# Optimization experiments

Hardware: AMD Instinct MI355X
Metric: run time of the kernel (lower is better)

Reference implementation:

```python
import jax, jax.numpy as jnp
import numpy as np

B, QL, ML = 8, 128, 1024
QS, KS, H = 512, 512, 256


def setup_inputs() -> dict:
    key = jax.random.key(0)
    ks = jax.random.split(key, 10)
    query = jax.random.normal(ks[0], (B, QL, QS), dtype=jnp.float32)
    memory = jax.random.normal(ks[1], (B, ML, KS), dtype=jnp.float32)
    mask = jax.random.bernoulli(ks[2], 0.1, (B, ML))
    mask = mask.at[:, 0].set(False)  # ensure at least one valid position per row
    s_q = 1.0 / np.sqrt(QS)
    s_k = 1.0 / np.sqrt(KS)
    s_h = 1.0 / np.sqrt(H)
    Wq = jax.random.uniform(ks[3], (H, QS), jnp.float32, -s_q, s_q)
    bq = jax.random.uniform(ks[4], (H,), jnp.float32, -s_q, s_q)
    Wk = jax.random.uniform(ks[5], (H, KS), jnp.float32, -s_k, s_k)
    bk = jax.random.uniform(ks[6], (H,), jnp.float32, -s_k, s_k)
    wl = jax.random.uniform(ks[7], (H,), jnp.float32, -s_h, s_h)
    bl = jax.random.uniform(ks[8], (), jnp.float32, -s_h, s_h)
    return {"query": query, "memory": memory, "mask": mask,
            "Wq": Wq, "bq": bq, "Wk": Wk, "bk": bk, "wl": wl, "bl": bl}


def reference(query, memory, mask, Wq, bq, Wk, bk, wl, bl):
    # q: [B, QL, H], k: [B, ML, H]
    q = jnp.einsum('bqs,hs->bqh', query, Wq) + bq
    k = jnp.einsum('bms,hs->bmh', memory, Wk) + bk
    # additive score: tanh(q + k) projected to scalar  -> [B, QL, ML]
    z = jnp.tanh(q[:, :, None, :] + k[:, None, :, :])  # [B, QL, ML, H]
    logits = jnp.einsum('bqmh,h->bqm', z, wl) + bl
    logits = jnp.where(mask[:, None, :], jnp.float32(-1e18), logits)
    weights = jax.nn.softmax(logits, axis=-1)  # BottleSoftmax over mem_len
    attns = jnp.einsum('bqm,bms->bqs', weights, memory)
    return attns, weights
```

## Files before the change

### kernel.cpp

```cpp
#include <hip/hip_runtime.h>

#define B_  8
#define QL_ 128
#define ML_ 1024
#define KS_ 512
#define H_  256

#define QP_OFF 0
#define KP_OFF 262144
#define MASK_OFF 2359296

__global__ __launch_bounds__(256) void proj_kernel(
    const float* __restrict__ query, const float* __restrict__ memory,
    const float* __restrict__ Wq, const float* __restrict__ bq,
    const float* __restrict__ Wk, const float* __restrict__ bk,
    float* __restrict__ Eq, float* __restrict__ Ek,
    const unsigned char* __restrict__ mraw, unsigned char* __restrict__ mout) {
    const int bid = blockIdx.x;
    const int t = threadIdx.x;

    if (bid == 576) {
        __shared__ int s_not01, s_not0f;
        const unsigned int* w = (const unsigned int*)mraw;
        if (t == 0) { s_not01 = 0; s_not0f = 0; }
        __syncthreads();
        int not01 = 0, not0f = 0;
        for (int i = t; i < 2048; i += 256) {
            unsigned int v = w[i];
            if (v != 0u && v != 1u) not01 = 1;
            if (v != 0u && v != 0x3F800000u) not0f = 1;
        }
        if (not01) atomicOr(&s_not01, 1);
        if (not0f) atomicOr(&s_not0f, 1);
        __syncthreads();
        int wordTyped = (!s_not01) || (!s_not0f);
        for (int i = t; i < B_ * ML_; i += 256) {
            unsigned char mv;
            if (wordTyped) mv = (w[i] != 0u) ? 1 : 0;
            else           mv = mraw[i] ? 1 : 0;
            mout[i] = mv;
        }
        return;
    }

    const float SC = 2.885390081777926815f;
    const int K = 512, N = 256;
    __shared__ float Xs[16][68];
    __shared__ float Ws[16][68];

    const float *X, *W, *bias; float* out; int bm, bn;
    if (bid < 64) { X = query;  W = Wq; bias = bq; out = Eq; bm = bid >> 2;        bn = bid & 3; }
    else          { X = memory; W = Wk; bias = bk; out = Ek; bm = (bid - 64) >> 2; bn = (bid - 64) & 3; }

    const int tx = t & 15, ty = t >> 4;
    const int lr = t >> 2;
    const int lk = (t & 3) << 2;
    const float* Xrow = X + (size_t)(bm * 64 + lr) * K + lk;
    const float* Wrow = W + (size_t)(bn * 64 + lr) * K + lk;
    float acc[4][4] = {};
    float4 xa = *(const float4*)(Xrow);
    float4 wa = *(const float4*)(Wrow);
    for (int k0 = 0; k0 < K; k0 += 16) {
        __syncthreads();
        Xs[lk + 0][lr] = xa.x; Xs[lk + 1][lr] = xa.y;
        Xs[lk + 2][lr] = xa.z; Xs[lk + 3][lr] = xa.w;
        Ws[lk + 0][lr] = wa.x; Ws[lk + 1][lr] = wa.y;
        Ws[lk + 2][lr] = wa.z; Ws[lk + 3][lr] = wa.w;
        __syncthreads();
        if (k0 + 16 < K) {
            xa = *(const float4*)(Xrow + k0 + 16);
            wa = *(const float4*)(Wrow + k0 + 16);
        }
#pragma unroll
        for (int k = 0; k < 16; ++k) {
            float4 av = *(const float4*)(&Xs[k][ty * 4]);
            float4 bv = *(const float4*)(&Ws[k][tx * 4]);
            float a[4] = {av.x, av.y, av.z, av.w};
            float b[4] = {bv.x, bv.y, bv.z, bv.w};
#pragma unroll
            for (int i = 0; i < 4; ++i)
#pragma unroll
                for (int j = 0; j < 4; ++j)
                    acc[i][j] = fmaf(a[i], b[j], acc[i][j]);
        }
    }
    float4 bv = *(const float4*)(bias + bn * 64 + tx * 4);
    float bvec[4] = {bv.x, bv.y, bv.z, bv.w};
#pragma unroll
    for (int i = 0; i < 4; ++i) {
        int m = bm * 64 + ty * 4 + i;
        float4 o;
        o.x = __builtin_amdgcn_exp2f(SC * (acc[i][0] + bvec[0]));
        o.y = __builtin_amdgcn_exp2f(SC * (acc[i][1] + bvec[1]));
        o.z = __builtin_amdgcn_exp2f(SC * (acc[i][2] + bvec[2]));
        o.w = __builtin_amdgcn_exp2f(SC * (acc[i][3] + bvec[3]));
        *(float4*)(out + (size_t)m * N + bn * 64 + tx * 4) = o;
    }
}

__global__ __launch_bounds__(256) void logits_kernel(
    const float* __restrict__ Eq, const float* __restrict__ Ek,
    const float* __restrict__ wl, float* __restrict__ sr) {
    const int bid = blockIdx.x;
    const int b  = bid & 7;
    const int r2 = bid >> 3;
    const int mt = r2 & 7;
    const int qt = r2 >> 3;
    const int tid = threadIdx.x;
    const int m  = tid & 127;
    const int qh = tid >> 7;

    __shared__ float eqs[2048];
    __shared__ float wls[256];
    __shared__ float kq[4][128][4];

    const float* qpb = Eq + ((size_t)(b * QL_ + qt * 8)) * H_;
    const float* kpb = Ek + ((size_t)(b * ML_ + mt * 128)) * H_;

    *(float4*)(&eqs[tid * 4])        = *(const float4*)(qpb + tid * 4);
    *(float4*)(&eqs[1024 + tid * 4]) = *(const float4*)(qpb + 1024 + tid * 4);
    if (tid < 64) *(float4*)(&wls[tid * 4]) = *(const float4*)(wl + tid * 4);

    const int srow = tid & 127;
    const int sq2  = tid >> 7;
    const float* kst = kpb + (size_t)srow * H_ + 8 * sq2;
    float4 a0 = *(const float4*)(kst);
    float4 a1 = *(const float4*)(kst + 4);

    float acc[4] = {0.f, 0.f, 0.f, 0.f};

    for (int c = 0; c < 16; ++c) {
        __syncthreads();
        *(float4*)(&kq[2 * sq2 + 0][srow][0]) = a0;
        *(float4*)(&kq[2 * sq2 + 1][srow][0]) = a1;
        __syncthreads();
        if (c < 15) {
            a0 = *(const float4*)(kst + (c + 1) * 16);
            a1 = *(const float4*)(kst + (c + 1) * 16 + 4);
        }
        const int h0 = c * 16;
#pragma unroll
        for (int quad = 0; quad < 4; ++quad) {
            float4 k4 = *(const float4*)(&kq[quad][m][0]);
            float4 w4 = *(const float4*)(&wls[h0 + quad * 4]);
#pragma unroll
            for (int j2 = 0; j2 < 4; ++j2) {
                float4 q4 = *(const float4*)(&eqs[(qh * 4 + j2) * 256 + h0 + quad * 4]);
                float p0 = fmaf(k4.x, q4.x, 1.0f);
                float p1 = fmaf(k4.y, q4.y, 1.0f);
                float p2 = fmaf(k4.z, q4.z, 1.0f);
                float p3 = fmaf(k4.w, q4.w, 1.0f);
                float p01 = p0 * p1, p23 = p2 * p3;
                float n01 = fmaf(w4.y, p0, w4.x * p1);
                float n23 = fmaf(w4.w, p2, w4.z * p3);
                float Nm  = fmaf(n23, p01, n01 * p23);
                float P   = p01 * p23;
                acc[j2] = fmaf(Nm, __builtin_amdgcn_rcpf(P), acc[j2]);
            }
        }
    }
#pragma unroll
    for (int j2 = 0; j2 < 4; ++j2)
        sr[((size_t)(b * QL_ + qt * 8 + qh * 4 + j2)) * ML_ + mt * 128 + m] = acc[j2];
}

__global__ __launch_bounds__(256) void softmax_kernel(
    float* __restrict__ wrow_io, const unsigned char* __restrict__ mv) {
    const int row = blockIdx.x;
    const int b = row >> 7;
    const int tid = threadIdx.x;
    float* srow = wrow_io + (size_t)row * ML_;
    const unsigned char* mrow = mv + b * ML_;
    __shared__ float red[4];

    float4 s4 = *(const float4*)(srow + tid * 4);
    uchar4 m4 = *(const uchar4*)(mrow + tid * 4);
    float l[4];
    l[0] = m4.x ? -1e18f : -2.0f * s4.x;
    l[1] = m4.y ? -1e18f : -2.0f * s4.y;
    l[2] = m4.z ? -1e18f : -2.0f * s4.z;
    l[3] = m4.w ? -1e18f : -2.0f * s4.w;

    float mx = fmaxf(fmaxf(l[0], l[1]), fmaxf(l[2], l[3]));
#pragma unroll
    for (int off = 32; off >= 1; off >>= 1)
        mx = fmaxf(mx, __shfl_xor(mx, off));
    if ((tid & 63) == 0) red[tid >> 6] = mx;
    __syncthreads();
    mx = fmaxf(fmaxf(red[0], red[1]), fmaxf(red[2], red[3]));
    __syncthreads();

    const float L2E = 1.44269504088896340736f;
    float e[4], s = 0.f;
#pragma unroll
    for (int i = 0; i < 4; ++i) {
        e[i] = __builtin_amdgcn_exp2f((l[i] - mx) * L2E);
        s += e[i];
    }
#pragma unroll
    for (int off = 32; off >= 1; off >>= 1)
        s += __shfl_xor(s, off);
    if ((tid & 63) == 0) red[tid >> 6] = s;
    __syncthreads();
    s = (red[0] + red[1]) + (red[2] + red[3]);
    float inv = __builtin_amdgcn_rcpf(s);
    float4 o = make_float4(e[0] * inv, e[1] * inv, e[2] * inv, e[3] * inv);
    *(float4*)(srow + tid * 4) = o;
}

__global__ __launch_bounds__(256) void attn_out_kernel(
    const float* __restrict__ wgt, const float* __restrict__ mem,
    float* __restrict__ out) {
    const int bid = blockIdx.x;
    const int b  = bid & 7;
    const int j2 = bid >> 3;
    const int mt = j2 & 3;
    const int nt = j2 >> 2;
    const int t = threadIdx.x;
    __shared__ float As[32][34];
    __shared__ float Bs[32][64];

    const int ar = t >> 3, ac = (t & 7) << 2;
    const int br = t >> 4, bc = (t & 15) << 2;
    const float* Ap = wgt + ((size_t)(b * QL_ + mt * 32 + ar)) * ML_ + ac;
    const float* Bp = mem + ((size_t)(b * ML_ + br)) * KS_ + nt * 64 + bc;

    const int tx = t & 15, ty = t >> 4;
    float acc0[4] = {0.f, 0.f, 0.f, 0.f};
    float acc1[4] = {0.f, 0.f, 0.f, 0.f};

    float4 apre = *(const float4*)(Ap);
    float4 bpre0 = *(const float4*)(Bp);
    float4 bpre1 = *(const float4*)(Bp + (size_t)16 * KS_);

    for (int k0 = 0; k0 < ML_; k0 += 32) {
        __syncthreads();
        As[ac + 0][ar] = apre.x; As[ac + 1][ar] = apre.y;
        As[ac + 2][ar] = apre.z; As[ac + 3][ar] = apre.w;
        *(float4*)(&Bs[br][bc])      = bpre0;
        *(float4*)(&Bs[br + 16][bc]) = bpre1;
        __syncthreads();
        if (k0 + 32 < ML_) {
            apre  = *(const float4*)(Ap + k0 + 32);
            bpre0 = *(const float4*)(Bp + (size_t)(k0 + 32) * KS_);
            bpre1 = *(const float4*)(Bp + (size_t)(k0 + 48) * KS_);
        }
#pragma unroll
        for (int kk = 0; kk < 32; ++kk) {
            float2 a2 = *(const float2*)(&As[kk][ty * 2]);
            float4 b4 = *(const float4*)(&Bs[kk][tx * 4]);
            acc0[0] = fmaf(a2.x, b4.x, acc0[0]);
            acc0[1] = fmaf(a2.x, b4.y, acc0[1]);
            acc0[2] = fmaf(a2.x, b4.z, acc0[2]);
            acc0[3] = fmaf(a2.x, b4.w, acc0[3]);
            acc1[0] = fmaf(a2.y, b4.x, acc1[0]);
            acc1[1] = fmaf(a2.y, b4.y, acc1[1]);
            acc1[2] = fmaf(a2.y, b4.z, acc1[2]);
            acc1[3] = fmaf(a2.y, b4.w, acc1[3]);
        }
    }
    size_t orow = ((size_t)(b * QL_ + mt * 32 + ty * 2)) * KS_ + nt * 64 + tx * 4;
    *(float4*)(out + orow)       = make_float4(acc0[0], acc0[1], acc0[2], acc0[3]);
    *(float4*)(out + orow + KS_) = make_float4(acc1[0], acc1[1], acc1[2], acc1[3]);
}

extern "C" void kernel_launch(void* const* d_in, const int* in_sizes, int n_in,
                              void* d_out, int out_size, void* d_ws, size_t ws_size,
                              hipStream_t stream) {
    const float* query  = (const float*)d_in[0];
    const float* memory = (const float*)d_in[1];
    const unsigned char* mask = (const unsigned char*)d_in[2];
    const float* Wq = (const float*)d_in[3];
    const float* bq = (const float*)d_in[4];
    const float* Wk = (const float*)d_in[5];
    const float* bk = (const float*)d_in[6];
    const float* wl = (const float*)d_in[7];

    float* ws = (float*)d_ws;
    float* Eq = ws + QP_OFF;
    float* Ek = ws + KP_OFF;
    unsigned char* mcan = (unsigned char*)(ws + MASK_OFF);

    float* attns = (float*)d_out;
    float* wout  = (float*)d_out + B_ * QL_ * KS_;

    proj_kernel<<<dim3(577), dim3(256), 0, stream>>>(query, memory, Wq, bq, Wk, bk,
                                                     Eq, Ek, mask, mcan);
    logits_kernel<<<dim3(1024), dim3(256), 0, stream>>>(Eq, Ek, wl, wout);
    softmax_kernel<<<dim3(B_ * QL_), dim3(256), 0, stream>>>(wout, mcan);
    attn_out_kernel<<<dim3(256), dim3(256), 0, stream>>>(wout, memory, attns);
}
```

Baseline: 190.9 us.

## Halve projection GEMM tile rows and double-buffer shared memory with K=32 chunks

```diff
diff --git a/kernel.cpp b/kernel.cpp
--- a/kernel.cpp
+++ b/kernel.cpp
@@ -19,7 +19,7 @@
     const int bid = blockIdx.x;
     const int t = threadIdx.x;
 
-    if (bid == 576) {
+    if (bid == 1152) {
         __shared__ int s_not01, s_not0f;
         const unsigned int* w = (const unsigned int*)mraw;
         if (t == 0) { s_not01 = 0; s_not0f = 0; }
@@ -45,50 +45,72 @@
 
     const float SC = 2.885390081777926815f;
     const int K = 512, N = 256;
-    __shared__ float Xs[16][68];
-    __shared__ float Ws[16][68];
+    __shared__ float Xs[2][32][34];
+    __shared__ float Ws[2][32][68];
 
     const float *X, *W, *bias; float* out; int bm, bn;
-    if (bid < 64) { X = query;  W = Wq; bias = bq; out = Eq; bm = bid >> 2;        bn = bid & 3; }
-    else          { X = memory; W = Wk; bias = bk; out = Ek; bm = (bid - 64) >> 2; bn = (bid - 64) & 3; }
+    if (bid < 128) { X = query;  W = Wq; bias = bq; out = Eq; bm = bid >> 2;         bn = bid & 3; }
+    else           { X = memory; W = Wk; bias = bk; out = Ek; bm = (bid - 128) >> 2; bn = (bid - 128) & 3; }
+
+    const int ar = t >> 3;
+    const int ak = (t & 7) << 2;
+    const float* Xrow  = X + (size_t)(bm * 32 + ar) * K + ak;
+    const float* Wrow0 = W + (size_t)(bn * 64 + ar) * K + ak;
+    const float* Wrow1 = W + (size_t)(bn * 64 + ar + 32) * K + ak;
 
     const int tx = t & 15, ty = t >> 4;
-    const int lr = t >> 2;
-    const int lk = (t & 3) << 2;
-    const float* Xrow = X + (size_t)(bm * 64 + lr) * K + lk;
-    const float* Wrow = W + (size_t)(bn * 64 + lr) * K + lk;
-    float acc[4][4] = {};
-    float4 xa = *(const float4*)(Xrow);
-    float4 wa = *(const float4*)(Wrow);
-    for (int k0 = 0; k0 < K; k0 += 16) {
-        __syncthreads();
-        Xs[lk + 0][lr] = xa.x; Xs[lk + 1][lr] = xa.y;
-        Xs[lk + 2][lr] = xa.z; Xs[lk + 3][lr] = xa.w;
-        Ws[lk + 0][lr] = wa.x; Ws[lk + 1][lr] = wa.y;
-        Ws[lk + 2][lr] = wa.z; Ws[lk + 3][lr] = wa.w;
-        __syncthreads();
-        if (k0 + 16 < K) {
-            xa = *(const float4*)(Xrow + k0 + 16);
-            wa = *(const float4*)(Wrow + k0 + 16);
-        }
-#pragma unroll
-        for (int k = 0; k < 16; ++k) {
-            float4 av = *(const float4*)(&Xs[k][ty * 4]);
-            float4 bv = *(const float4*)(&Ws[k][tx * 4]);
-            float a[4] = {av.x, av.y, av.z, av.w};
-            float b[4] = {bv.x, bv.y, bv.z, bv.w};
-#pragma unroll
-            for (int i = 0; i < 4; ++i)
-#pragma unroll
-                for (int j = 0; j < 4; ++j)
-                    acc[i][j] = fmaf(a[i], b[j], acc[i][j]);
-        }
-    }
+    float acc[2][4] = {};
+
+    float4 xa  = *(const float4*)(Xrow);
+    float4 wa0 = *(const float4*)(Wrow0);
+    float4 wa1 = *(const float4*)(Wrow1);
+    Xs[0][ak + 0][ar] = xa.x;  Xs[0][ak + 1][ar] = xa.y;
+    Xs[0][ak + 2][ar] = xa.z;  Xs[0][ak + 3][ar] = xa.w;
+    Ws[0][ak + 0][ar] = wa0.x; Ws[0][ak + 1][ar] = wa0.y;
+    Ws[0][ak + 2][ar] = wa0.z; Ws[0][ak + 3][ar] = wa0.w;
+    Ws[0][ak + 0][ar + 32] = wa1.x; Ws[0][ak + 1][ar + 32] = wa1.y;
+    Ws[0][ak + 2][ar + 32] = wa1.z; Ws[0][ak + 3][ar + 32] = wa1.w;
+    xa  = *(const float4*)(Xrow + 32);
+    wa0 = *(const float4*)(Wrow0 + 32);
+    wa1 = *(const float4*)(Wrow1 + 32);
+    __syncthreads();
+
+    for (int c = 0; c < 16; ++c) {
+        const int p = c & 1;
+        if (c < 15) {
+            Xs[p ^ 1][ak + 0][ar] = xa.x;  Xs[p ^ 1][ak + 1][ar] = xa.y;
+            Xs[p ^ 1][ak + 2][ar] = xa.z;  Xs[p ^ 1][ak + 3][ar] = xa.w;
+            Ws[p ^ 1][ak + 0][ar] = wa0.x; Ws[p ^ 1][ak + 1][ar] = wa0.y;
+            Ws[p ^ 1][ak + 2][ar] = wa0.z; Ws[p ^ 1][ak + 3][ar] = wa0.w;
+            Ws[p ^ 1][ak + 0][ar + 32] = wa1.x; Ws[p ^ 1][ak + 1][ar + 32] = wa1.y;
+            Ws[p ^ 1][ak + 2][ar + 32] = wa1.z; Ws[p ^ 1][ak + 3][ar + 32] = wa1.w;
+            if (c < 14) {
+                xa  = *(const float4*)(Xrow  + (c + 2) * 32);
+                wa0 = *(const float4*)(Wrow0 + (c + 2) * 32);
+                wa1 = *(const float4*)(Wrow1 + (c + 2) * 32);
+            }
+        }
+#pragma unroll
+        for (int k = 0; k < 32; ++k) {
+            float2 a2 = *(const float2*)(&Xs[p][k][ty * 2]);
+            float4 b4 = *(const float4*)(&Ws[p][k][tx * 4]);
+            acc[0][0] = fmaf(a2.x, b4.x, acc[0][0]);
+            acc[0][1] = fmaf(a2.x, b4.y, acc[0][1]);
+            acc[0][2] = fmaf(a2.x, b4.z, acc[0][2]);
+            acc[0][3] = fmaf(a2.x, b4.w, acc[0][3]);
+            acc[1][0] = fmaf(a2.y, b4.x, acc[1][0]);
+            acc[1][1] = fmaf(a2.y, b4.y, acc[1][1]);
+            acc[1][2] = fmaf(a2.y, b4.z, acc[1][2]);
+            acc[1][3] = fmaf(a2.y, b4.w, acc[1][3]);
+        }
+        __syncthreads();
+    }
+
     float4 bv = *(const float4*)(bias + bn * 64 + tx * 4);
     float bvec[4] = {bv.x, bv.y, bv.z, bv.w};
 #pragma unroll
-    for (int i = 0; i < 4; ++i) {
-        int m = bm * 64 + ty * 4 + i;
+    for (int i = 0; i < 2; ++i) {
+        int m = bm * 32 + ty * 2 + i;
         float4 o;
         o.x = __builtin_amdgcn_exp2f(SC * (acc[i][0] + bvec[0]));
         o.y = __builtin_amdgcn_exp2f(SC * (acc[i][1] + bvec[1]));
@@ -284,8 +306,8 @@
     float* attns = (float*)d_out;
     float* wout  = (float*)d_out + B_ * QL_ * KS_;
 
-    proj_kernel<<<dim3(577), dim3(256), 0, stream>>>(query, memory, Wq, bq, Wk, bk,
-                                                     Eq, Ek, mask, mcan);
+    proj_kernel<<<dim3(1153), dim3(256), 0, stream>>>(query, memory, Wq, bq, Wk, bk,
+                                                      Eq, Ek, mask, mcan);
     logits_kernel<<<dim3(1024), dim3(256), 0, stream>>>(Eq, Ek, wl, wout);
     softmax_kernel<<<dim3(B_ * QL_), dim3(256), 0, stream>>>(wout, mcan);
     attn_out_kernel<<<dim3(256), dim3(256), 0, stream>>>(wout, memory, attns);
```

Result: slower. 201.2 us (+5.4%).

## Compute Q/K projections with split-bf16 MFMA instead of FP32 FMA tiles

Applied to the files above, without the earlier changes.

```diff
diff --git a/kernel.cpp b/kernel.cpp
--- a/kernel.cpp
+++ b/kernel.cpp
@@ -10,7 +10,25 @@
 #define KP_OFF 262144
 #define MASK_OFF 2359296
 
-__global__ __launch_bounds__(256) void proj_kernel(
+typedef __attribute__((ext_vector_type(8))) short bfrag;
+typedef __attribute__((ext_vector_type(4))) float f4acc;
+
+__device__ __forceinline__ void split8(const float4& a, const float4& b,
+                                       bfrag& hi, bfrag& lo) {
+    const float v[8] = {a.x, a.y, a.z, a.w, b.x, b.y, b.z, b.w};
+#pragma unroll
+    for (int j = 0; j < 8; ++j) {
+        unsigned u  = __float_as_uint(v[j]);
+        unsigned hb = u & 0xFFFF0000u;
+        float    lf = v[j] - __uint_as_float(hb);
+        unsigned ul = __float_as_uint(lf);
+        unsigned lr = ul + 0x7FFFu + ((ul >> 16) & 1u);
+        hi[j] = (short)(u >> 16);
+        lo[j] = (short)(lr >> 16);
+    }
+}
+
+__global__ __launch_bounds__(256, 1) void proj_kernel(
     const float* __restrict__ query, const float* __restrict__ memory,
     const float* __restrict__ Wq, const float* __restrict__ bq,
     const float* __restrict__ Wk, const float* __restrict__ bk,
@@ -19,7 +37,7 @@
     const int bid = blockIdx.x;
     const int t = threadIdx.x;
 
-    if (bid == 576) {
+    if (bid == 144) {
         __shared__ int s_not01, s_not0f;
         const unsigned int* w = (const unsigned int*)mraw;
         if (t == 0) { s_not01 = 0; s_not0f = 0; }
@@ -45,57 +63,86 @@
 
     const float SC = 2.885390081777926815f;
     const int K = 512, N = 256;
-    __shared__ float Xs[16][68];
-    __shared__ float Ws[16][68];
-
-    const float *X, *W, *bias; float* out; int bm, bn;
-    if (bid < 64) { X = query;  W = Wq; bias = bq; out = Eq; bm = bid >> 2;        bn = bid & 3; }
-    else          { X = memory; W = Wk; bias = bk; out = Ek; bm = (bid - 64) >> 2; bn = (bid - 64) & 3; }
-
-    const int tx = t & 15, ty = t >> 4;
-    const int lr = t >> 2;
-    const int lk = (t & 3) << 2;
-    const float* Xrow = X + (size_t)(bm * 64 + lr) * K + lk;
-    const float* Wrow = W + (size_t)(bn * 64 + lr) * K + lk;
-    float acc[4][4] = {};
-    float4 xa = *(const float4*)(Xrow);
-    float4 wa = *(const float4*)(Wrow);
-    for (int k0 = 0; k0 < K; k0 += 16) {
-        __syncthreads();
-        Xs[lk + 0][lr] = xa.x; Xs[lk + 1][lr] = xa.y;
-        Xs[lk + 2][lr] = xa.z; Xs[lk + 3][lr] = xa.w;
-        Ws[lk + 0][lr] = wa.x; Ws[lk + 1][lr] = wa.y;
-        Ws[lk + 2][lr] = wa.z; Ws[lk + 3][lr] = wa.w;
-        __syncthreads();
-        if (k0 + 16 < K) {
-            xa = *(const float4*)(Xrow + k0 + 16);
-            wa = *(const float4*)(Wrow + k0 + 16);
-        }
-#pragma unroll
-        for (int k = 0; k < 16; ++k) {
-            float4 av = *(const float4*)(&Xs[k][ty * 4]);
-            float4 bv = *(const float4*)(&Ws[k][tx * 4]);
-            float a[4] = {av.x, av.y, av.z, av.w};
-            float b[4] = {bv.x, bv.y, bv.z, bv.w};
-#pragma unroll
-            for (int i = 0; i < 4; ++i)
-#pragma unroll
-                for (int j = 0; j < 4; ++j)
-                    acc[i][j] = fmaf(a[i], b[j], acc[i][j]);
-        }
-    }
-    float4 bv = *(const float4*)(bias + bn * 64 + tx * 4);
-    float bvec[4] = {bv.x, bv.y, bv.z, bv.w};
+
+    const float *X, *W, *bias; float* out; int bm;
+    if (bid < 16) { X = query;  W = Wq; bias = bq; out = Eq; bm = bid; }
+    else          { X = memory; W = Wk; bias = bk; out = Ek; bm = bid - 16; }
+
+    const int w  = t >> 6;
+    const int l  = t & 63;
+    const int lr = l & 15;
+    const int lk = l >> 4;
+
+    const float* Arow[4];
+    const float* Brow[4];
 #pragma unroll
     for (int i = 0; i < 4; ++i) {
-        int m = bm * 64 + ty * 4 + i;
-        float4 o;
-        o.x = __builtin_amdgcn_exp2f(SC * (acc[i][0] + bvec[0]));
-        o.y = __builtin_amdgcn_exp2f(SC * (acc[i][1] + bvec[1]));
-        o.z = __builtin_amdgcn_exp2f(SC * (acc[i][2] + bvec[2]));
-        o.w = __builtin_amdgcn_exp2f(SC * (acc[i][3] + bvec[3]));
-        *(float4*)(out + (size_t)m * N + bn * 64 + tx * 4) = o;
-    }
+        Arow[i] = X + (size_t)(bm * 64 + i * 16 + lr) * K + lk * 8;
+        Brow[i] = W + (size_t)(w * 64 + i * 16 + lr) * K + lk * 8;
+    }
+
+    f4acc acc[4][4];
+#pragma unroll
+    for (int mi = 0; mi < 4; ++mi)
+#pragma unroll
+        for (int ni = 0; ni < 4; ++ni)
+            acc[mi][ni] = (f4acc){0.f, 0.f, 0.f, 0.f};
+
+    float4 p0a[4][2], p0b[4][2], p1a[4][2], p1b[4][2];
+
+#define LOADC(Pa, Pb, c) do {                                        \
+    _Pragma("unroll")                                                \
+    for (int i = 0; i < 4; ++i) {                                    \
+        Pa[i][0] = *(const float4*)(Arow[i] + (c) * 32);             \
+        Pa[i][1] = *(const float4*)(Arow[i] + (c) * 32 + 4);         \
+        Pb[i][0] = *(const float4*)(Brow[i] + (c) * 32);             \
+        Pb[i][1] = *(const float4*)(Brow[i] + (c) * 32 + 4);         \
+    } } while (0)
+
+#define COMPUTE(Pa, Pb) do {                                                   \
+    bfrag ahi[4], alo[4], bhi[4], blo[4];                                      \
+    _Pragma("unroll")                                                          \
+    for (int i = 0; i < 4; ++i) split8(Pa[i][0], Pa[i][1], ahi[i], alo[i]);    \
+    _Pragma("unroll")                                                          \
+    for (int i = 0; i < 4; ++i) split8(Pb[i][0], Pb[i][1], bhi[i], blo[i]);    \
+    _Pragma("unroll")                                                          \
+    for (int mi = 0; mi < 4; ++mi)                                             \
+    _Pragma("unroll")                                                          \
+    for (int ni = 0; ni < 4; ++ni) {                                           \
+        acc[mi][ni] = __builtin_amdgcn_mfma_f32_16x16x32_bf16(                 \
+            ahi[mi], bhi[ni], acc[mi][ni], 0, 0, 0);                           \
+        acc[mi][ni] = __builtin_amdgcn_mfma_f32_16x16x32_bf16(                 \
+            ahi[mi], blo[ni], acc[mi][ni], 0, 0, 0);                           \
+        acc[mi][ni] = __builtin_amdgcn_mfma_f32_16x16x32_bf16(                 \
+            alo[mi], bhi[ni], acc[mi][ni], 0, 0, 0);                           \
+    } } while (0)
+
+    LOADC(p0a, p0b, 0);
+    for (int c2 = 0; c2 < 8; ++c2) {
+        LOADC(p1a, p1b, 2 * c2 + 1);
+        COMPUTE(p0a, p0b);
+        if (c2 < 7) LOADC(p0a, p0b, 2 * c2 + 2);
+        COMPUTE(p1a, p1b);
+    }
+#undef LOADC
+#undef COMPUTE
+
+    float bcol[4];
+#pragma unroll
+    for (int ni = 0; ni < 4; ++ni) bcol[ni] = bias[w * 64 + ni * 16 + lr];
+
+#pragma unroll
+    for (int mi = 0; mi < 4; ++mi)
+#pragma unroll
+        for (int ni = 0; ni < 4; ++ni) {
+            const int col = w * 64 + ni * 16 + lr;
+#pragma unroll
+            for (int r = 0; r < 4; ++r) {
+                const int row = bm * 64 + mi * 16 + lk * 4 + r;
+                out[(size_t)row * N + col] =
+                    __builtin_amdgcn_exp2f(SC * (acc[mi][ni][r] + bcol[ni]));
+            }
+        }
 }
 
 __global__ __launch_bounds__(256) void logits_kernel(
@@ -284,7 +331,7 @@
     float* attns = (float*)d_out;
     float* wout  = (float*)d_out + B_ * QL_ * KS_;
 
-    proj_kernel<<<dim3(577), dim3(256), 0, stream>>>(query, memory, Wq, bq, Wk, bk,
+    proj_kernel<<<dim3(145), dim3(256), 0, stream>>>(query, memory, Wq, bq, Wk, bk,
                                                      Eq, Ek, mask, mcan);
     logits_kernel<<<dim3(1024), dim3(256), 0, stream>>>(Eq, Ek, wl, wout);
     softmax_kernel<<<dim3(B_ * QL_), dim3(256), 0, stream>>>(wout, mcan);
```

Result: faster. 180.1 us (-5.7%).

## Move projection GEMMs to bf16x3 split MFMA with pre-split weights

Applied to the files above, without the earlier changes.

```diff
diff --git a/kernel.cpp b/kernel.cpp
--- a/kernel.cpp
+++ b/kernel.cpp
@@ -9,17 +9,39 @@
 #define QP_OFF 0
 #define KP_OFF 262144
 #define MASK_OFF 2359296
-
-__global__ __launch_bounds__(256) void proj_kernel(
-    const float* __restrict__ query, const float* __restrict__ memory,
-    const float* __restrict__ Wq, const float* __restrict__ bq,
-    const float* __restrict__ Wk, const float* __restrict__ bk,
-    float* __restrict__ Eq, float* __restrict__ Ek,
+#define WH_OFF 2361344
+#define WL_OFF 2492416
+
+typedef __attribute__((ext_vector_type(8))) short bfrag;
+typedef __attribute__((ext_vector_type(4))) float f4acc;
+
+__device__ __forceinline__ void split1(float v, unsigned& h, unsigned& lo) {
+    unsigned u  = __float_as_uint(v);
+    unsigned hb = u & 0xFFFF0000u;
+    float    lf = v - __uint_as_float(hb);
+    unsigned ul = __float_as_uint(lf);
+    unsigned lr = ul + 0x7FFFu + ((ul >> 16) & 1u);
+    h  = u >> 16;
+    lo = lr >> 16;
+}
+
+__device__ __forceinline__ void split4(const float4& a, unsigned& h01, unsigned& h23,
+                                       unsigned& l01, unsigned& l23) {
+    unsigned h[4], l[4];
+    split1(a.x, h[0], l[0]); split1(a.y, h[1], l[1]);
+    split1(a.z, h[2], l[2]); split1(a.w, h[3], l[3]);
+    h01 = h[0] | (h[1] << 16); h23 = h[2] | (h[3] << 16);
+    l01 = l[0] | (l[1] << 16); l23 = l[2] | (l[3] << 16);
+}
+
+__global__ __launch_bounds__(256) void prep_kernel(
+    const float* __restrict__ Wq, const float* __restrict__ Wk,
+    unsigned short* __restrict__ Whi, unsigned short* __restrict__ Wlo,
     const unsigned char* __restrict__ mraw, unsigned char* __restrict__ mout) {
     const int bid = blockIdx.x;
     const int t = threadIdx.x;
 
-    if (bid == 576) {
+    if (bid == 64) {
         __shared__ int s_not01, s_not0f;
         const unsigned int* w = (const unsigned int*)mraw;
         if (t == 0) { s_not01 = 0; s_not0f = 0; }
@@ -43,59 +65,146 @@
         return;
     }
 
+    const float* src = (bid < 32) ? Wq : Wk;
+    const int lb = bid & 31;
+    const size_t loff = (size_t)lb * 4096 + (size_t)t * 16;
+    const size_t doff = ((bid < 32) ? 0 : 131072) + loff;
+
+    unsigned hw[8], lw[8];
+#pragma unroll
+    for (int i = 0; i < 4; ++i) {
+        float4 v = *(const float4*)(src + loff + i * 4);
+        split4(v, hw[i * 2], hw[i * 2 + 1], lw[i * 2], lw[i * 2 + 1]);
+    }
+    *(uint4*)(Whi + doff)     = make_uint4(hw[0], hw[1], hw[2], hw[3]);
+    *(uint4*)(Whi + doff + 8) = make_uint4(hw[4], hw[5], hw[6], hw[7]);
+    *(uint4*)(Wlo + doff)     = make_uint4(lw[0], lw[1], lw[2], lw[3]);
+    *(uint4*)(Wlo + doff + 8) = make_uint4(lw[4], lw[5], lw[6], lw[7]);
+}
+
+__global__ __launch_bounds__(256) void proj_kernel(
+    const float* __restrict__ query, const float* __restrict__ memory,
+    const unsigned short* __restrict__ Whi, const unsigned short* __restrict__ Wlo,
+    const float* __restrict__ bq, const float* __restrict__ bk,
+    float* __restrict__ Eq, float* __restrict__ Ek) {
+    const int bid = blockIdx.x;
+    const int t = threadIdx.x;
+    const int nb = bid & 1;
+    const int mb = bid >> 1;
+
+    const float *X, *bias; float* out; int row0, wbase0;
+    if (mb < 32) { X = query;  bias = bq; out = Eq; row0 = mb * 32;        wbase0 = 0; }
+    else         { X = memory; bias = bk; out = Ek; row0 = (mb - 32) * 32; wbase0 = 256; }
+
+    const int w  = t >> 6;
+    const int l  = t & 63;
+    const int lr = l & 15;
+    const int lk = l >> 4;
+
+    const int arow = t >> 3;
+    const int acol = (t & 7) << 2;
+    const float* Xp = X + (size_t)(row0 + arow) * 512 + acol;
+    __shared__ unsigned int AH[2][32][16];
+    __shared__ unsigned int AL[2][32][16];
+    const int wg  = ((t & 7) >> 1) ^ ((arow >> 1) & 3);
+    const int wwo = ((t & 7) & 1) << 1;
+
+    const int wrow0 = wbase0 + nb * 128 + w * 32;
+    const unsigned short* bhP0 = Whi + (size_t)(wrow0 + 0 * 16 + lr) * 512 + lk * 8;
+    const unsigned short* bhP1 = Whi + (size_t)(wrow0 + 1 * 16 + lr) * 512 + lk * 8;
+    const unsigned short* blP0 = Wlo + (size_t)(wrow0 + 0 * 16 + lr) * 512 + lk * 8;
+    const unsigned short* blP1 = Wlo + (size_t)(wrow0 + 1 * 16 + lr) * 512 + lk * 8;
+
+    f4acc acc[2][2];
+#pragma unroll
+    for (int mi = 0; mi < 2; ++mi)
+#pragma unroll
+        for (int ni = 0; ni < 2; ++ni)
+            acc[mi][ni] = (f4acc){0.f, 0.f, 0.f, 0.f};
+
+#define WRA(P, XA) do {                                               \
+    unsigned h01, h23, l01, l23;                                      \
+    split4(XA, h01, h23, l01, l23);                                   \
+    unsigned int* dh = &AH[P][arow][wg * 4 + wwo];                    \
+    unsigned int* dl = &AL[P][arow][wg * 4 + wwo];                    \
+    dh[0] = h01; dh[1] = h23; dl[0] = l01; dl[1] = l23; } while (0)
+
+#define LDB(BH0, BH1, BL0, BL1, c) do {                               \
+    BH0 = *(const uint4*)(bhP0 + (size_t)(c) * 32);                   \
+    BH1 = *(const uint4*)(bhP1 + (size_t)(c) * 32);                   \
+    BL0 = *(const uint4*)(blP0 + (size_t)(c) * 32);                   \
+    BL1 = *(const uint4*)(blP1 + (size_t)(c) * 32); } while (0)
+
+#define COMP(P, BH0, BH1, BL0, BL1) do {                              \
+    bfrag ah[2], al[2];                                               \
+    _Pragma("unroll")                                                 \
+    for (int mi = 0; mi < 2; ++mi) {                                  \
+        int ra = mi * 16 + lr;                                        \
+        int g4 = (lk ^ ((ra >> 1) & 3)) * 4;                          \
+        ah[mi] = *(const bfrag*)&AH[P][ra][g4];                       \
+        al[mi] = *(const bfrag*)&AL[P][ra][g4];                       \
+    }                                                                 \
+    bfrag bh[2], bl[2];                                               \
+    bh[0] = __builtin_bit_cast(bfrag, BH0);                           \
+    bh[1] = __builtin_bit_cast(bfrag, BH1);                           \
+    bl[0] = __builtin_bit_cast(bfrag, BL0);                           \
+    bl[1] = __builtin_bit_cast(bfrag, BL1);                           \
+    _Pragma("unroll")                                                 \
+    for (int mi = 0; mi < 2; ++mi)                                    \
+    _Pragma("unroll")                                                 \
+    for (int ni = 0; ni < 2; ++ni) {                                  \
+        acc[mi][ni] = __builtin_amdgcn_mfma_f32_16x16x32_bf16(        \
+            ah[mi], bh[ni], acc[mi][ni], 0, 0, 0);                    \
+        acc[mi][ni] = __builtin_amdgcn_mfma_f32_16x16x32_bf16(        \
+            ah[mi], bl[ni], acc[mi][ni], 0, 0, 0);                    \
+        acc[mi][ni] = __builtin_amdgcn_mfma_f32_16x16x32_bf16(        \
+            al[mi], bh[ni], acc[mi][ni], 0, 0, 0);                    \
+    } } while (0)
+
+    float4 xa0 = *(const float4*)(Xp);
+    uint4 bh00, bh01, bl00, bl01;
+    LDB(bh00, bh01, bl00, bl01, 0);
+    float4 xa1 = *(const float4*)(Xp + 32);
+    uint4 bh10, bh11, bl10, bl11;
+    LDB(bh10, bh11, bl10, bl11, 1);
+    WRA(0, xa0);
+    __syncthreads();
+
+    for (int c2 = 0; c2 < 8; ++c2) {
+        WRA(1, xa1);
+        if (c2 < 7) xa0 = *(const float4*)(Xp + (2 * c2 + 2) * 32);
+        COMP(0, bh00, bh01, bl00, bl01);
+        if (c2 < 7) LDB(bh00, bh01, bl00, bl01, 2 * c2 + 2);
+        __syncthreads();
+        if (c2 < 7) WRA(0, xa0);
+        COMP(1, bh10, bh11, bl10, bl11);
+        if (c2 < 7) {
+            xa1 = *(const float4*)(Xp + (2 * c2 + 3) * 32);
+            LDB(bh10, bh11, bl10, bl11, 2 * c2 + 3);
+        }
+        __syncthreads();
+    }
+#undef WRA
+#undef LDB
+#undef COMP
+
     const float SC = 2.885390081777926815f;
-    const int K = 512, N = 256;
-    __shared__ float Xs[16][68];
-    __shared__ float Ws[16][68];
-
-    const float *X, *W, *bias; float* out; int bm, bn;
-    if (bid < 64) { X = query;  W = Wq; bias = bq; out = Eq; bm = bid >> 2;        bn = bid & 3; }
-    else          { X = memory; W = Wk; bias = bk; out = Ek; bm = (bid - 64) >> 2; bn = (bid - 64) & 3; }
-
-    const int tx = t & 15, ty = t >> 4;
-    const int lr = t >> 2;
-    const int lk = (t & 3) << 2;
-    const float* Xrow = X + (size_t)(bm * 64 + lr) * K + lk;
-    const float* Wrow = W + (size_t)(bn * 64 + lr) * K + lk;
-    float acc[4][4] = {};
-    float4 xa = *(const float4*)(Xrow);
-    float4 wa = *(const float4*)(Wrow);
-    for (int k0 = 0; k0 < K; k0 += 16) {
-        __syncthreads();
-        Xs[lk + 0][lr] = xa.x; Xs[lk + 1][lr] = xa.y;
-        Xs[lk + 2][lr] = xa.z; Xs[lk + 3][lr] = xa.w;
-        Ws[lk + 0][lr] = wa.x; Ws[lk + 1][lr] = wa.y;
-        Ws[lk + 2][lr] = wa.z; Ws[lk + 3][lr] = wa.w;
-        __syncthreads();
-        if (k0 + 16 < K) {
-            xa = *(const float4*)(Xrow + k0 + 16);
-            wa = *(const float4*)(Wrow + k0 + 16);
-        }
-#pragma unroll
-        for (int k = 0; k < 16; ++k) {
-            float4 av = *(const float4*)(&Xs[k][ty * 4]);
-            float4 bv = *(const float4*)(&Ws[k][tx * 4]);
-            float a[4] = {av.x, av.y, av.z, av.w};
-            float b[4] = {bv.x, bv.y, bv.z, bv.w};
-#pragma unroll
-            for (int i = 0; i < 4; ++i)
-#pragma unroll
-                for (int j = 0; j < 4; ++j)
-                    acc[i][j] = fmaf(a[i], b[j], acc[i][j]);
-        }
-    }
-    float4 bv = *(const float4*)(bias + bn * 64 + tx * 4);
-    float bvec[4] = {bv.x, bv.y, bv.z, bv.w};
-#pragma unroll
-    for (int i = 0; i < 4; ++i) {
-        int m = bm * 64 + ty * 4 + i;
-        float4 o;
-        o.x = __builtin_amdgcn_exp2f(SC * (acc[i][0] + bvec[0]));
-        o.y = __builtin_amdgcn_exp2f(SC * (acc[i][1] + bvec[1]));
-        o.z = __builtin_amdgcn_exp2f(SC * (acc[i][2] + bvec[2]));
-        o.w = __builtin_amdgcn_exp2f(SC * (acc[i][3] + bvec[3]));
-        *(float4*)(out + (size_t)m * N + bn * 64 + tx * 4) = o;
-    }
+    float bcol[2];
+#pragma unroll
+    for (int ni = 0; ni < 2; ++ni) bcol[ni] = bias[nb * 128 + w * 32 + ni * 16 + lr];
+
+#pragma unroll
+    for (int mi = 0; mi < 2; ++mi)
+#pragma unroll
+        for (int ni = 0; ni < 2; ++ni) {
+            const int col = nb * 128 + w * 32 + ni * 16 + lr;
+#pragma unroll
+            for (int r = 0; r < 4; ++r) {
+                const int row = row0 + mi * 16 + lk * 4 + r;
+                out[(size_t)row * 256 + col] =
+                    __builtin_amdgcn_exp2f(SC * (acc[mi][ni][r] + bcol[ni]));
+            }
+        }
 }
 
 __global__ __launch_bounds__(256) void logits_kernel(
@@ -280,12 +389,15 @@
     float* Eq = ws + QP_OFF;
     float* Ek = ws + KP_OFF;
     unsigned char* mcan = (unsigned char*)(ws + MASK_OFF);
+    unsigned short* Whi = (unsigned short*)(ws + WH_OFF);
+    unsigned short* Wlo = (unsigned short*)(ws + WL_OFF);
 
     float* attns = (float*)d_out;
     float* wout  = (float*)d_out + B_ * QL_ * KS_;
 
-    proj_kernel<<<dim3(577), dim3(256), 0, stream>>>(query, memory, Wq, bq, Wk, bk,
-                                                     Eq, Ek, mask, mcan);
+    prep_kernel<<<dim3(65),  dim3(256), 0, stream>>>(Wq, Wk, Whi, Wlo, mask, mcan);
+    proj_kernel<<<dim3(576), dim3(256), 0, stream>>>(query, memory, Whi, Wlo,
+                                                     bq, bk, Eq, Ek);
     logits_kernel<<<dim3(1024), dim3(256), 0, stream>>>(Eq, Ek, wl, wout);
     softmax_kernel<<<dim3(B_ * QL_), dim3(256), 0, stream>>>(wout, mcan);
     attn_out_kernel<<<dim3(256), dim3(256), 0, stream>>>(wout, memory, attns);
```

New measurement: 187.1 us. 2.0% less time.
